# Performance work log

Measured on AMD Instinct MI355X. Metric: run time of the kernel, lower is better.

Reference implementation:

```python
import jax, jax.numpy as jnp
import numpy as np

N_CLASSES = 5
N_SAMPLES = 512
D_EMB = 512


def setup_inputs() -> dict:
    key = jax.random.key(0)
    k1, k2, k3 = jax.random.split(key, 3)
    prediction = jax.random.normal(k1, (N_SAMPLES, D_EMB), dtype=jnp.float32)
    target = jax.random.randint(k2, (N_SAMPLES,), 0, N_CLASSES)
    # learnable_map=None -> all learnable, init = inverse_softplus(0.5 + 0.5*U[0,1))
    t = 0.5 + 0.5 * jax.random.uniform(k3, (N_CLASSES - 1,), dtype=jnp.float32)
    distances_raw = jnp.log(jnp.exp(t) - 1.0)  # inverse softplus (t < 20 always)
    return {"prediction": prediction, "distances_raw": distances_raw, "target": target}


def reference(prediction, distances_raw, target):
    n = prediction.shape[0]
    eps = 1e-8  # torch F.cosine_similarity eps
    xn = prediction / jnp.maximum(jnp.linalg.norm(prediction, axis=1, keepdims=True), eps)
    cos = xn @ xn.T  # [i, j] pairwise cosine similarity

    same = target[:, None] == target[None, :]          # label_diff <= 0
    positives = same & ~jnp.eye(n, dtype=bool)          # same label, not self
    negatives = ~same                                   # different label

    # ordinal class positions from softplus-parameterized gaps
    pos_d = jax.nn.softplus(distances_raw)
    class_pos = jnp.concatenate([jnp.zeros(1, dtype=pos_d.dtype), jnp.cumsum(pos_d)])
    cp = class_pos[target]
    margins = jnp.where(negatives, jnp.abs(cp[:, None] - cp[None, :]), 0.0)  # [i, j]

    # Original loop over anchor-positive columns k:
    #   n_pair_loss[k][i, j] = -cos[i, k] + cos[i, j] + margins[i, j]
    #   valid iff positives[i, k] and negatives[i, j]; invalid -> relu(-inf)=0
    base = cos + margins                                # [i, j]
    diff = base[:, None, :] - cos[:, :, None]           # [i, k, j]
    val = jnp.where(negatives[:, None, :], jax.nn.relu(diff), 0.0)
    s = jnp.where(positives, val.sum(axis=2), 0.0)      # [i, k]
    negcount = negatives.sum(axis=1)                    # [i]
    cnt = jnp.where(positives, negcount[:, None], 0)    # loss_mask2
    L = s / jnp.maximum(cnt, 1)                         # per (anchor i, positive k)

    # mean over nonzero entries (mean_n_pair_loss[mean_n_pair_loss != 0].mean())
    nz = (L != 0.0).sum()
    return L.sum() / jnp.maximum(nz, 1).astype(L.dtype)
```

## Files before the change

kernel.cpp:

```cpp
#include <hip/hip_runtime.h>
#include <math.h>

#define NS 512
#define DE 512
#define NCL 5
#define KSPLIT 16
#define PART_ELEMS (KSPLIT * NS * NS)


__global__ __launch_bounds__(256, 1) void k_gemm(const float* __restrict__ pred,
                                                 float* __restrict__ part,
                                                 float* __restrict__ dpart,
                                                 unsigned int* __restrict__ ctrl) {
    const int tid = threadIdx.x;
    if (blockIdx.x == 0 && blockIdx.y == 0 && blockIdx.z == 0 && tid < 4) ctrl[tid] = 0u;

    __shared__ float4 As4[128][8];
    __shared__ float4 Bs4[128][8];

    const int row0 = blockIdx.y * 128, col0 = blockIdx.x * 128;
    const int z = blockIdx.z;
    const int kz0 = z * 32;

    const int lr = tid >> 1;
    const int sbase = (tid & 1) * 4;
    const int swz = (lr >> 3) & 7;
    const float4* gA = (const float4*)&pred[(row0 + lr) * DE + kz0];
    const float4* gB = (const float4*)&pred[(col0 + lr) * DE + kz0];
#pragma unroll
    for (int q = 0; q < 4; q++) {
        int s = sbase + q;
        As4[lr][s ^ swz] = gA[s];
        Bs4[lr][s ^ swz] = gB[s];
    }
    __syncthreads();

    const int tx = tid & 15, ty = tid >> 4;
    const int aswz = ty & 7, bswz = tx & 7;
    float acc[8][8] = {};

#pragma unroll
    for (int q = 0; q < 8; q++) {
        float4 b4[8];
#pragma unroll
        for (int c = 0; c < 8; c++) b4[c] = Bs4[tx * 8 + c][q ^ bswz];
#pragma unroll
        for (int rr = 0; rr < 2; rr++) {
            float4 a4[4];
#pragma unroll
            for (int r = 0; r < 4; r++) a4[r] = As4[ty * 8 + rr * 4 + r][q ^ aswz];
#pragma unroll
            for (int r = 0; r < 4; r++) {
#pragma unroll
                for (int c = 0; c < 8; c++) {
                    float v = acc[rr * 4 + r][c];
                    v = fmaf(a4[r].x, b4[c].x, v);
                    v = fmaf(a4[r].y, b4[c].y, v);
                    v = fmaf(a4[r].z, b4[c].z, v);
                    v = fmaf(a4[r].w, b4[c].w, v);
                    acc[rr * 4 + r][c] = v;
                }
            }
        }
    }

    float* op = part + (size_t)z * NS * NS;
#pragma unroll
    for (int m = 0; m < 8; m++) {
        float4 o0 = make_float4(acc[m][0], acc[m][1], acc[m][2], acc[m][3]);
        float4 o1 = make_float4(acc[m][4], acc[m][5], acc[m][6], acc[m][7]);
        float* dst = &op[(row0 + ty * 8 + m) * NS + col0 + tx * 8];
        *(float4*)dst = o0;
        *(float4*)(dst + 4) = o1;
    }

    if (blockIdx.x == blockIdx.y && ty == tx) {
#pragma unroll
        for (int m = 0; m < 8; m++)
            dpart[z * NS + row0 + ty * 8 + m] = acc[m][m];
    }
}

__global__ __launch_bounds__(256) void k_loss(const float* __restrict__ part,
                                              const float* __restrict__ dpart,
                                              const int* __restrict__ target,
                                              const float* __restrict__ draw,
                                              unsigned int* __restrict__ ctrl,
                                              float* __restrict__ out) {
    const int b = blockIdx.x;
    const int tid = threadIdx.x;
    const int iA = b, iB = b + 256;

    __shared__ float4 v4sA[NS / 4], v4sB[NS / 4];
    __shared__ float  ckA[NS], ckB[NS];
    __shared__ float  rn_s[NS];
    __shared__ int    pkA[NS], pkB[NS];
    __shared__ float  spart[NS * 17];
    __shared__ float  redf[256];
    __shared__ int    redi[256];
    __shared__ unsigned int pcA, pcB;

    float* gsum = (float*)ctrl;
    unsigned int* gnz    = ctrl + 1;
    unsigned int* ticket = ctrl + 2;

    float2 d2 = make_float2(0.0f, 0.0f);
#pragma unroll
    for (int z = 0; z < KSPLIT; z++) {
        float2 t2 = ((const float2*)&dpart[z * NS])[tid];
        d2.x += t2.x; d2.y += t2.y;
    }
    const float rn0 = 1.0f / fmaxf(sqrtf(d2.x), 1e-8f);
    const float rn1 = 1.0f / fmaxf(sqrtf(d2.y), 1e-8f);
    const int j0 = tid * 2;
    rn_s[j0] = rn0; rn_s[j0 + 1] = rn1;
    if (tid == 0) { pcA = 0u; pcB = 0u; }

    float2 gA = make_float2(0.0f, 0.0f), gB = make_float2(0.0f, 0.0f);
#pragma unroll
    for (int z = 0; z < KSPLIT; z++) {
        const float* base = part + (size_t)z * NS * NS;
        float2 tA = ((const float2*)&base[(size_t)iA * NS])[tid];
        float2 tB = ((const float2*)&base[(size_t)iB * NS])[tid];
        gA.x += tA.x; gA.y += tA.y;
        gB.x += tB.x; gB.y += tB.y;
    }

    float cp[NCL];
    cp[0] = 0.0f;
#pragma unroll
    for (int c = 0; c < NCL - 1; c++) cp[c + 1] = cp[c] + log1pf(expf(draw[c]));
    const int tiA = target[iA], tiB = target[iB];
    const float cpA = cp[tiA], cpB = cp[tiB];
    __syncthreads();

    const float rniA = rn_s[iA], rniB = rn_s[iB];
    const int tj0 = target[j0], tj1 = target[j0 + 1];
    const float cpj0 = cp[tj0], cpj1 = cp[tj1];

    {
        float c0 = gA.x * rniA * rn0;
        float c1 = gA.y * rniA * rn1;
        bool n0 = (tj0 != tiA), n1 = (tj1 != tiA);
        ckA[j0] = c0; ckA[j0 + 1] = c1;
        ((float2*)v4sA)[tid] = make_float2(n0 ? (c0 + fabsf(cpA - cpj0)) : -1e30f,
                                           n1 ? (c1 + fabsf(cpA - cpj1)) : -1e30f);
        if (!n0 && j0 != iA)     pkA[atomicAdd(&pcA, 1u)] = j0;
        if (!n1 && j0 + 1 != iA) pkA[atomicAdd(&pcA, 1u)] = j0 + 1;
        redi[tid] = ((n0 ? 1 : 0) + (n1 ? 1 : 0));
    }
    {
        float c0 = gB.x * rniB * rn0;
        float c1 = gB.y * rniB * rn1;
        bool n0 = (tj0 != tiB), n1 = (tj1 != tiB);
        ckB[j0] = c0; ckB[j0 + 1] = c1;
        ((float2*)v4sB)[tid] = make_float2(n0 ? (c0 + fabsf(cpB - cpj0)) : -1e30f,
                                           n1 ? (c1 + fabsf(cpB - cpj1)) : -1e30f);
        if (!n0 && j0 != iB)     pkB[atomicAdd(&pcB, 1u)] = j0;
        if (!n1 && j0 + 1 != iB) pkB[atomicAdd(&pcB, 1u)] = j0 + 1;
        redi[tid] += ((n0 ? 1 : 0) + (n1 ? 1 : 0)) << 16;
    }
    __syncthreads();
    for (int s = 128; s > 0; s >>= 1) {
        if (tid < s) redi[tid] += redi[tid + s];
        __syncthreads();
    }
    const int negA = redi[0] & 0xffff;
    const int negB = redi[0] >> 16;
    const unsigned int nposA = pcA, nposB = pcB;
    __syncthreads();

    const int kl = tid & 15, jc = tid >> 4;
    const float denA = (float)(negA > 1 ? negA : 1);
    const float denB = (float)(negB > 1 ? negB : 1);
    float contrib = 0.0f;
    int nzc = 0;

    {
        float4 vj[8];
#pragma unroll
        for (int t = 0; t < 8; t++) vj[t] = v4sA[jc * 8 + t];
        for (unsigned int p = kl; p < nposA; p += 16) {
            const float ckp = ckA[pkA[p]];
            float s0 = 0.0f, s1 = 0.0f;
#pragma unroll
            for (int t = 0; t < 8; t++) {
                float4 w = vj[t];
                s0 += fmaxf(w.x - ckp, 0.0f) + fmaxf(w.y - ckp, 0.0f);
                s1 += fmaxf(w.z - ckp, 0.0f) + fmaxf(w.w - ckp, 0.0f);
            }
            spart[p * 17 + jc] = s0 + s1;
        }
        __syncthreads();
        for (unsigned int p = tid; p < nposA; p += 256) {
            float s = 0.0f;
#pragma unroll
            for (int q = 0; q < 16; q++) s += spart[p * 17 + q];
            contrib += s / denA;
            if (s != 0.0f) nzc++;
        }
        __syncthreads();
    }
    {
        float4 vj[8];
#pragma unroll
        for (int t = 0; t < 8; t++) vj[t] = v4sB[jc * 8 + t];
        for (unsigned int p = kl; p < nposB; p += 16) {
            const float ckp = ckB[pkB[p]];
            float s0 = 0.0f, s1 = 0.0f;
#pragma unroll
            for (int t = 0; t < 8; t++) {
                float4 w = vj[t];
                s0 += fmaxf(w.x - ckp, 0.0f) + fmaxf(w.y - ckp, 0.0f);
                s1 += fmaxf(w.z - ckp, 0.0f) + fmaxf(w.w - ckp, 0.0f);
            }
            spart[p * 17 + jc] = s0 + s1;
        }
        __syncthreads();
        for (unsigned int p = tid; p < nposB; p += 256) {
            float s = 0.0f;
#pragma unroll
            for (int q = 0; q < 16; q++) s += spart[p * 17 + q];
            contrib += s / denB;
            if (s != 0.0f) nzc++;
        }
    }

    redf[tid] = contrib;
    redi[tid] = nzc;
    __syncthreads();
    for (int s = 128; s > 0; s >>= 1) {
        if (tid < s) { redf[tid] += redf[tid + s]; redi[tid] += redi[tid + s]; }
        __syncthreads();
    }
    if (tid == 0) {
        if (redf[0] != 0.0f || redi[0] != 0) {
            atomicAdd(gsum, redf[0]);
            atomicAdd(gnz, (unsigned int)redi[0]);
        }
        __threadfence();
        unsigned int t = atomicAdd(ticket, 1u);
        if (t == (unsigned int)(gridDim.x - 1)) {
            float s = atomicAdd(gsum, 0.0f);
            unsigned int n = atomicAdd(gnz, 0u);
            out[0] = s / (float)(n > 1u ? n : 1u);
        }
    }
}

extern "C" void kernel_launch(void* const* d_in, const int* in_sizes, int n_in,
                              void* d_out, int out_size, void* d_ws, size_t ws_size,
                              hipStream_t stream) {
    const float* pred   = (const float*)d_in[0];
    const float* draw   = (const float*)d_in[1];
    const int*   target = (const int*)d_in[2];
    float* out = (float*)d_out;

    float* ws    = (float*)d_ws;
    float* part  = ws;
    float* dpart = ws + PART_ELEMS;
    unsigned int* ctrl = (unsigned int*)(dpart + KSPLIT * NS);

    hipLaunchKernelGGL(k_gemm, dim3(4, 4, KSPLIT), dim3(256), 0, stream,
                       pred, part, dpart, ctrl);
    hipLaunchKernelGGL(k_loss, dim3(256), dim3(256), 0, stream,
                       part, dpart, target, draw, ctrl, out);
}
```

Baseline: 91.22 us.

## Fuse GEMM and loss kernels with a software grid barrier

```diff
diff --git a/kernel.cpp b/kernel.cpp
--- a/kernel.cpp
+++ b/kernel.cpp
@@ -6,103 +6,113 @@
 #define NCL 5
 #define KSPLIT 16
 #define PART_ELEMS (KSPLIT * NS * NS)
-
-
-__global__ __launch_bounds__(256, 1) void k_gemm(const float* __restrict__ pred,
-                                                 float* __restrict__ part,
-                                                 float* __restrict__ dpart,
-                                                 unsigned int* __restrict__ ctrl) {
+#define NBLK 256
+
+
+union SMem {
+    struct { float4 As4[128][8]; float4 Bs4[128][8]; } g;
+    struct {
+        float4 v4sA[NS / 4], v4sB[NS / 4];
+        float  ckA[NS], ckB[NS];
+        float  rn_s[NS];
+        int    pkA[NS], pkB[NS];
+        float  spart[NS * 17];
+        float  redf[256];
+        int    redi[256];
+        unsigned int pcA, pcB;
+    } l;
+};
+
+__global__ __launch_bounds__(256) void k_fused(const float* __restrict__ pred,
+                                               const int* __restrict__ target,
+                                               const float* __restrict__ draw,
+                                               float* __restrict__ part,
+                                               float* __restrict__ dpart,
+                                               unsigned int* __restrict__ ctrl,
+                                               float* __restrict__ out) {
+    __shared__ SMem sm;
     const int tid = threadIdx.x;
-    if (blockIdx.x == 0 && blockIdx.y == 0 && blockIdx.z == 0 && tid < 4) ctrl[tid] = 0u;
-
-    __shared__ float4 As4[128][8];
-    __shared__ float4 Bs4[128][8];
-
-    const int row0 = blockIdx.y * 128, col0 = blockIdx.x * 128;
-    const int z = blockIdx.z;
-    const int kz0 = z * 32;
-
-    const int lr = tid >> 1;
-    const int sbase = (tid & 1) * 4;
-    const int swz = (lr >> 3) & 7;
-    const float4* gA = (const float4*)&pred[(row0 + lr) * DE + kz0];
-    const float4* gB = (const float4*)&pred[(col0 + lr) * DE + kz0];
-#pragma unroll
-    for (int q = 0; q < 4; q++) {
-        int s = sbase + q;
-        As4[lr][s ^ swz] = gA[s];
-        Bs4[lr][s ^ swz] = gB[s];
-    }
-    __syncthreads();
-
-    const int tx = tid & 15, ty = tid >> 4;
-    const int aswz = ty & 7, bswz = tx & 7;
-    float acc[8][8] = {};
-
-#pragma unroll
-    for (int q = 0; q < 8; q++) {
-        float4 b4[8];
-#pragma unroll
-        for (int c = 0; c < 8; c++) b4[c] = Bs4[tx * 8 + c][q ^ bswz];
-#pragma unroll
-        for (int rr = 0; rr < 2; rr++) {
-            float4 a4[4];
-#pragma unroll
-            for (int r = 0; r < 4; r++) a4[r] = As4[ty * 8 + rr * 4 + r][q ^ aswz];
-#pragma unroll
-            for (int r = 0; r < 4; r++) {
-#pragma unroll
-                for (int c = 0; c < 8; c++) {
-                    float v = acc[rr * 4 + r][c];
-                    v = fmaf(a4[r].x, b4[c].x, v);
-                    v = fmaf(a4[r].y, b4[c].y, v);
-                    v = fmaf(a4[r].z, b4[c].z, v);
-                    v = fmaf(a4[r].w, b4[c].w, v);
-                    acc[rr * 4 + r][c] = v;
+    const int b = blockIdx.x;
+
+    {
+        const int t = b >> 4, z = b & 15;
+        const int row0 = (t >> 2) * 128, col0 = (t & 3) * 128;
+        const int kz0 = z * 32;
+
+        const int lr = tid >> 1;
+        const int sbase = (tid & 1) * 4;
+        const int swz = (lr >> 3) & 7;
+        const float4* gA = (const float4*)&pred[(row0 + lr) * DE + kz0];
+        const float4* gB = (const float4*)&pred[(col0 + lr) * DE + kz0];
+#pragma unroll
+        for (int q = 0; q < 4; q++) {
+            int s = sbase + q;
+            sm.g.As4[lr][s ^ swz] = gA[s];
+            sm.g.Bs4[lr][s ^ swz] = gB[s];
+        }
+        __syncthreads();
+
+        const int tx = tid & 15, ty = tid >> 4;
+        const int aswz = ty & 7, bswz = tx & 7;
+        float acc[8][8] = {};
+#pragma unroll
+        for (int q = 0; q < 8; q++) {
+            float4 b4[8];
+#pragma unroll
+            for (int c = 0; c < 8; c++) b4[c] = sm.g.Bs4[tx * 8 + c][q ^ bswz];
+#pragma unroll
+            for (int rr = 0; rr < 2; rr++) {
+                float4 a4[4];
+#pragma unroll
+                for (int r = 0; r < 4; r++) a4[r] = sm.g.As4[ty * 8 + rr * 4 + r][q ^ aswz];
+#pragma unroll
+                for (int r = 0; r < 4; r++) {
+#pragma unroll
+                    for (int c = 0; c < 8; c++) {
+                        float v = acc[rr * 4 + r][c];
+                        v = fmaf(a4[r].x, b4[c].x, v);
+                        v = fmaf(a4[r].y, b4[c].y, v);
+                        v = fmaf(a4[r].z, b4[c].z, v);
+                        v = fmaf(a4[r].w, b4[c].w, v);
+                        acc[rr * 4 + r][c] = v;
+                    }
                 }
             }
         }
-    }
-
-    float* op = part + (size_t)z * NS * NS;
-#pragma unroll
-    for (int m = 0; m < 8; m++) {
-        float4 o0 = make_float4(acc[m][0], acc[m][1], acc[m][2], acc[m][3]);
-        float4 o1 = make_float4(acc[m][4], acc[m][5], acc[m][6], acc[m][7]);
-        float* dst = &op[(row0 + ty * 8 + m) * NS + col0 + tx * 8];
-        *(float4*)dst = o0;
-        *(float4*)(dst + 4) = o1;
-    }
-
-    if (blockIdx.x == blockIdx.y && ty == tx) {
-#pragma unroll
-        for (int m = 0; m < 8; m++)
-            dpart[z * NS + row0 + ty * 8 + m] = acc[m][m];
-    }
-}
-
-__global__ __launch_bounds__(256) void k_loss(const float* __restrict__ part,
-                                              const float* __restrict__ dpart,
-                                              const int* __restrict__ target,
-                                              const float* __restrict__ draw,
-                                              unsigned int* __restrict__ ctrl,
-                                              float* __restrict__ out) {
-    const int b = blockIdx.x;
-    const int tid = threadIdx.x;
+        float* op = part + (size_t)z * NS * NS;
+#pragma unroll
+        for (int m = 0; m < 8; m++) {
+            float4 o0 = make_float4(acc[m][0], acc[m][1], acc[m][2], acc[m][3]);
+            float4 o1 = make_float4(acc[m][4], acc[m][5], acc[m][6], acc[m][7]);
+            float* dst = &op[(row0 + ty * 8 + m) * NS + col0 + tx * 8];
+            *(float4*)dst = o0;
+            *(float4*)(dst + 4) = o1;
+        }
+        if ((t >> 2) == (t & 3) && ty == tx) {
+#pragma unroll
+            for (int m = 0; m < 8; m++)
+                dpart[z * NS + row0 + ty * 8 + m] = acc[m][m];
+        }
+    }
+
+    {
+        __threadfence();
+        __syncthreads();
+        if (tid == 0) {
+            unsigned int* bar = ctrl + 2;
+            atomicAdd(bar, 1u);
+            while (__hip_atomic_load(bar, __ATOMIC_ACQUIRE,
+                                     __HIP_MEMORY_SCOPE_AGENT) < (unsigned int)NBLK)
+                __builtin_amdgcn_s_sleep(4);
+        }
+        __syncthreads();
+        __threadfence();
+    }
+
     const int iA = b, iB = b + 256;
-
-    __shared__ float4 v4sA[NS / 4], v4sB[NS / 4];
-    __shared__ float  ckA[NS], ckB[NS];
-    __shared__ float  rn_s[NS];
-    __shared__ int    pkA[NS], pkB[NS];
-    __shared__ float  spart[NS * 17];
-    __shared__ float  redf[256];
-    __shared__ int    redi[256];
-    __shared__ unsigned int pcA, pcB;
-
     float* gsum = (float*)ctrl;
     unsigned int* gnz    = ctrl + 1;
-    unsigned int* ticket = ctrl + 2;
+    unsigned int* ticket = ctrl + 3;
 
     float2 d2 = make_float2(0.0f, 0.0f);
 #pragma unroll
@@ -113,17 +123,17 @@
     const float rn0 = 1.0f / fmaxf(sqrtf(d2.x), 1e-8f);
     const float rn1 = 1.0f / fmaxf(sqrtf(d2.y), 1e-8f);
     const int j0 = tid * 2;
-    rn_s[j0] = rn0; rn_s[j0 + 1] = rn1;
-    if (tid == 0) { pcA = 0u; pcB = 0u; }
-
-    float2 gA = make_float2(0.0f, 0.0f), gB = make_float2(0.0f, 0.0f);
+    sm.l.rn_s[j0] = rn0; sm.l.rn_s[j0 + 1] = rn1;
+    if (tid == 0) { sm.l.pcA = 0u; sm.l.pcB = 0u; }
+
+    float2 gA2 = make_float2(0.0f, 0.0f), gB2 = make_float2(0.0f, 0.0f);
 #pragma unroll
     for (int z = 0; z < KSPLIT; z++) {
         const float* base = part + (size_t)z * NS * NS;
         float2 tA = ((const float2*)&base[(size_t)iA * NS])[tid];
         float2 tB = ((const float2*)&base[(size_t)iB * NS])[tid];
-        gA.x += tA.x; gA.y += tA.y;
-        gB.x += tB.x; gB.y += tB.y;
+        gA2.x += tA.x; gA2.y += tA.y;
+        gB2.x += tB.x; gB2.y += tB.y;
     }
 
     float cp[NCL];
@@ -134,40 +144,40 @@
     const float cpA = cp[tiA], cpB = cp[tiB];
     __syncthreads();
 
-    const float rniA = rn_s[iA], rniB = rn_s[iB];
+    const float rniA = sm.l.rn_s[iA], rniB = sm.l.rn_s[iB];
     const int tj0 = target[j0], tj1 = target[j0 + 1];
     const float cpj0 = cp[tj0], cpj1 = cp[tj1];
 
     {
-        float c0 = gA.x * rniA * rn0;
-        float c1 = gA.y * rniA * rn1;
+        float c0 = gA2.x * rniA * rn0;
+        float c1 = gA2.y * rniA * rn1;
         bool n0 = (tj0 != tiA), n1 = (tj1 != tiA);
-        ckA[j0] = c0; ckA[j0 + 1] = c1;
-        ((float2*)v4sA)[tid] = make_float2(n0 ? (c0 + fabsf(cpA - cpj0)) : -1e30f,
-                                           n1 ? (c1 + fabsf(cpA - cpj1)) : -1e30f);
-        if (!n0 && j0 != iA)     pkA[atomicAdd(&pcA, 1u)] = j0;
-        if (!n1 && j0 + 1 != iA) pkA[atomicAdd(&pcA, 1u)] = j0 + 1;
-        redi[tid] = ((n0 ? 1 : 0) + (n1 ? 1 : 0));
-    }
-    {
-        float c0 = gB.x * rniB * rn0;
-        float c1 = gB.y * rniB * rn1;
+        sm.l.ckA[j0] = c0; sm.l.ckA[j0 + 1] = c1;
+        ((float2*)sm.l.v4sA)[tid] = make_float2(n0 ? (c0 + fabsf(cpA - cpj0)) : -1e30f,
+                                                n1 ? (c1 + fabsf(cpA - cpj1)) : -1e30f);
+        if (!n0 && j0 != iA)     sm.l.pkA[atomicAdd(&sm.l.pcA, 1u)] = j0;
+        if (!n1 && j0 + 1 != iA) sm.l.pkA[atomicAdd(&sm.l.pcA, 1u)] = j0 + 1;
+        sm.l.redi[tid] = ((n0 ? 1 : 0) + (n1 ? 1 : 0));
+    }
+    {
+        float c0 = gB2.x * rniB * rn0;
+        float c1 = gB2.y * rniB * rn1;
         bool n0 = (tj0 != tiB), n1 = (tj1 != tiB);
-        ckB[j0] = c0; ckB[j0 + 1] = c1;
-        ((float2*)v4sB)[tid] = make_float2(n0 ? (c0 + fabsf(cpB - cpj0)) : -1e30f,
-                                           n1 ? (c1 + fabsf(cpB - cpj1)) : -1e30f);
-        if (!n0 && j0 != iB)     pkB[atomicAdd(&pcB, 1u)] = j0;
-        if (!n1 && j0 + 1 != iB) pkB[atomicAdd(&pcB, 1u)] = j0 + 1;
-        redi[tid] += ((n0 ? 1 : 0) + (n1 ? 1 : 0)) << 16;
+        sm.l.ckB[j0] = c0; sm.l.ckB[j0 + 1] = c1;
+        ((float2*)sm.l.v4sB)[tid] = make_float2(n0 ? (c0 + fabsf(cpB - cpj0)) : -1e30f,
+                                                n1 ? (c1 + fabsf(cpB - cpj1)) : -1e30f);
+        if (!n0 && j0 != iB)     sm.l.pkB[atomicAdd(&sm.l.pcB, 1u)] = j0;
+        if (!n1 && j0 + 1 != iB) sm.l.pkB[atomicAdd(&sm.l.pcB, 1u)] = j0 + 1;
+        sm.l.redi[tid] += ((n0 ? 1 : 0) + (n1 ? 1 : 0)) << 16;
     }
     __syncthreads();
     for (int s = 128; s > 0; s >>= 1) {
-        if (tid < s) redi[tid] += redi[tid + s];
-        __syncthreads();
-    }
-    const int negA = redi[0] & 0xffff;
-    const int negB = redi[0] >> 16;
-    const unsigned int nposA = pcA, nposB = pcB;
+        if (tid < s) sm.l.redi[tid] += sm.l.redi[tid + s];
+        __syncthreads();
+    }
+    const int negA = sm.l.redi[0] & 0xffff;
+    const int negB = sm.l.redi[0] >> 16;
+    const unsigned int nposA = sm.l.pcA, nposB = sm.l.pcB;
     __syncthreads();
 
     const int kl = tid & 15, jc = tid >> 4;
@@ -179,9 +189,9 @@
     {
         float4 vj[8];
 #pragma unroll
-        for (int t = 0; t < 8; t++) vj[t] = v4sA[jc * 8 + t];
+        for (int t = 0; t < 8; t++) vj[t] = sm.l.v4sA[jc * 8 + t];
         for (unsigned int p = kl; p < nposA; p += 16) {
-            const float ckp = ckA[pkA[p]];
+            const float ckp = sm.l.ckA[sm.l.pkA[p]];
             float s0 = 0.0f, s1 = 0.0f;
 #pragma unroll
             for (int t = 0; t < 8; t++) {
@@ -189,13 +199,13 @@
                 s0 += fmaxf(w.x - ckp, 0.0f) + fmaxf(w.y - ckp, 0.0f);
                 s1 += fmaxf(w.z - ckp, 0.0f) + fmaxf(w.w - ckp, 0.0f);
             }
-            spart[p * 17 + jc] = s0 + s1;
+            sm.l.spart[p * 17 + jc] = s0 + s1;
         }
         __syncthreads();
         for (unsigned int p = tid; p < nposA; p += 256) {
             float s = 0.0f;
 #pragma unroll
-            for (int q = 0; q < 16; q++) s += spart[p * 17 + q];
+            for (int q = 0; q < 16; q++) s += sm.l.spart[p * 17 + q];
             contrib += s / denA;
             if (s != 0.0f) nzc++;
         }
@@ -204,9 +214,9 @@
     {
         float4 vj[8];
 #pragma unroll
-        for (int t = 0; t < 8; t++) vj[t] = v4sB[jc * 8 + t];
+        for (int t = 0; t < 8; t++) vj[t] = sm.l.v4sB[jc * 8 + t];
         for (unsigned int p = kl; p < nposB; p += 16) {
-            const float ckp = ckB[pkB[p]];
+            const float ckp = sm.l.ckB[sm.l.pkB[p]];
             float s0 = 0.0f, s1 = 0.0f;
 #pragma unroll
             for (int t = 0; t < 8; t++) {
@@ -214,33 +224,33 @@
                 s0 += fmaxf(w.x - ckp, 0.0f) + fmaxf(w.y - ckp, 0.0f);
                 s1 += fmaxf(w.z - ckp, 0.0f) + fmaxf(w.w - ckp, 0.0f);
             }
-            spart[p * 17 + jc] = s0 + s1;
+            sm.l.spart[p * 17 + jc] = s0 + s1;
         }
         __syncthreads();
         for (unsigned int p = tid; p < nposB; p += 256) {
             float s = 0.0f;
 #pragma unroll
-            for (int q = 0; q < 16; q++) s += spart[p * 17 + q];
+            for (int q = 0; q < 16; q++) s += sm.l.spart[p * 17 + q];
             contrib += s / denB;
             if (s != 0.0f) nzc++;
         }
     }
 
-    redf[tid] = contrib;
-    redi[tid] = nzc;
+    sm.l.redf[tid] = contrib;
+    sm.l.redi[tid] = nzc;
     __syncthreads();
     for (int s = 128; s > 0; s >>= 1) {
-        if (tid < s) { redf[tid] += redf[tid + s]; redi[tid] += redi[tid + s]; }
+        if (tid < s) { sm.l.redf[tid] += sm.l.redf[tid + s]; sm.l.redi[tid] += sm.l.redi[tid + s]; }
         __syncthreads();
     }
     if (tid == 0) {
-        if (redf[0] != 0.0f || redi[0] != 0) {
-            atomicAdd(gsum, redf[0]);
-            atomicAdd(gnz, (unsigned int)redi[0]);
+        if (sm.l.redf[0] != 0.0f || sm.l.redi[0] != 0) {
+            atomicAdd(gsum, sm.l.redf[0]);
+            atomicAdd(gnz, (unsigned int)sm.l.redi[0]);
         }
         __threadfence();
         unsigned int t = atomicAdd(ticket, 1u);
-        if (t == (unsigned int)(gridDim.x - 1)) {
+        if (t == (unsigned int)(NBLK - 1)) {
             float s = atomicAdd(gsum, 0.0f);
             unsigned int n = atomicAdd(gnz, 0u);
             out[0] = s / (float)(n > 1u ? n : 1u);
@@ -261,8 +271,7 @@
     float* dpart = ws + PART_ELEMS;
     unsigned int* ctrl = (unsigned int*)(dpart + KSPLIT * NS);
 
-    hipLaunchKernelGGL(k_gemm, dim3(4, 4, KSPLIT), dim3(256), 0, stream,
-                       pred, part, dpart, ctrl);
-    hipLaunchKernelGGL(k_loss, dim3(256), dim3(256), 0, stream,
-                       part, dpart, target, draw, ctrl, out);
+    hipMemsetAsync(ctrl, 0, 4 * sizeof(unsigned int), stream);
+    hipLaunchKernelGGL(k_fused, dim3(NBLK), dim3(256), 0, stream,
+                       pred, target, draw, part, dpart, ctrl, out);
 }
```

Measured after the change: 156.1 us. 71.2% more time.

## Fuse split-K GEMM into loss kernel computing cosine rows per block

Applied to the files above, without the earlier changes.

```diff
diff --git a/kernel.cpp b/kernel.cpp
--- a/kernel.cpp
+++ b/kernel.cpp
@@ -4,96 +4,22 @@
 #define NS 512
 #define DE 512
 #define NCL 5
-#define KSPLIT 16
-#define PART_ELEMS (KSPLIT * NS * NS)
-
-
-__global__ __launch_bounds__(256, 1) void k_gemm(const float* __restrict__ pred,
-                                                 float* __restrict__ part,
-                                                 float* __restrict__ dpart,
-                                                 unsigned int* __restrict__ ctrl) {
-    const int tid = threadIdx.x;
-    if (blockIdx.x == 0 && blockIdx.y == 0 && blockIdx.z == 0 && tid < 4) ctrl[tid] = 0u;
-
-    __shared__ float4 As4[128][8];
-    __shared__ float4 Bs4[128][8];
-
-    const int row0 = blockIdx.y * 128, col0 = blockIdx.x * 128;
-    const int z = blockIdx.z;
-    const int kz0 = z * 32;
-
-    const int lr = tid >> 1;
-    const int sbase = (tid & 1) * 4;
-    const int swz = (lr >> 3) & 7;
-    const float4* gA = (const float4*)&pred[(row0 + lr) * DE + kz0];
-    const float4* gB = (const float4*)&pred[(col0 + lr) * DE + kz0];
-#pragma unroll
-    for (int q = 0; q < 4; q++) {
-        int s = sbase + q;
-        As4[lr][s ^ swz] = gA[s];
-        Bs4[lr][s ^ swz] = gB[s];
-    }
-    __syncthreads();
-
-    const int tx = tid & 15, ty = tid >> 4;
-    const int aswz = ty & 7, bswz = tx & 7;
-    float acc[8][8] = {};
-
-#pragma unroll
-    for (int q = 0; q < 8; q++) {
-        float4 b4[8];
-#pragma unroll
-        for (int c = 0; c < 8; c++) b4[c] = Bs4[tx * 8 + c][q ^ bswz];
-#pragma unroll
-        for (int rr = 0; rr < 2; rr++) {
-            float4 a4[4];
-#pragma unroll
-            for (int r = 0; r < 4; r++) a4[r] = As4[ty * 8 + rr * 4 + r][q ^ aswz];
-#pragma unroll
-            for (int r = 0; r < 4; r++) {
-#pragma unroll
-                for (int c = 0; c < 8; c++) {
-                    float v = acc[rr * 4 + r][c];
-                    v = fmaf(a4[r].x, b4[c].x, v);
-                    v = fmaf(a4[r].y, b4[c].y, v);
-                    v = fmaf(a4[r].z, b4[c].z, v);
-                    v = fmaf(a4[r].w, b4[c].w, v);
-                    acc[rr * 4 + r][c] = v;
-                }
-            }
-        }
-    }
-
-    float* op = part + (size_t)z * NS * NS;
-#pragma unroll
-    for (int m = 0; m < 8; m++) {
-        float4 o0 = make_float4(acc[m][0], acc[m][1], acc[m][2], acc[m][3]);
-        float4 o1 = make_float4(acc[m][4], acc[m][5], acc[m][6], acc[m][7]);
-        float* dst = &op[(row0 + ty * 8 + m) * NS + col0 + tx * 8];
-        *(float4*)dst = o0;
-        *(float4*)(dst + 4) = o1;
-    }
-
-    if (blockIdx.x == blockIdx.y && ty == tx) {
-#pragma unroll
-        for (int m = 0; m < 8; m++)
-            dpart[z * NS + row0 + ty * 8 + m] = acc[m][m];
-    }
-}
-
-__global__ __launch_bounds__(256) void k_loss(const float* __restrict__ part,
-                                              const float* __restrict__ dpart,
-                                              const int* __restrict__ target,
-                                              const float* __restrict__ draw,
-                                              unsigned int* __restrict__ ctrl,
-                                              float* __restrict__ out) {
+#define NBLK 256
+
+
+__global__ __launch_bounds__(256) void k_all(const float* __restrict__ pred,
+                                             const int* __restrict__ target,
+                                             const float* __restrict__ draw,
+                                             unsigned int* __restrict__ ctrl,
+                                             float* __restrict__ out) {
     const int b = blockIdx.x;
     const int tid = threadIdx.x;
     const int iA = b, iB = b + 256;
 
+    __shared__ float4 sA4[DE / 4], sB4[DE / 4];
+    __shared__ float  rn_s[NS];
     __shared__ float4 v4sA[NS / 4], v4sB[NS / 4];
     __shared__ float  ckA[NS], ckB[NS];
-    __shared__ float  rn_s[NS];
     __shared__ int    pkA[NS], pkB[NS];
     __shared__ float  spart[NS * 17];
     __shared__ float  redf[256];
@@ -104,27 +30,44 @@
     unsigned int* gnz    = ctrl + 1;
     unsigned int* ticket = ctrl + 2;
 
-    float2 d2 = make_float2(0.0f, 0.0f);
-#pragma unroll
-    for (int z = 0; z < KSPLIT; z++) {
-        float2 t2 = ((const float2*)&dpart[z * NS])[tid];
-        d2.x += t2.x; d2.y += t2.y;
-    }
-    const float rn0 = 1.0f / fmaxf(sqrtf(d2.x), 1e-8f);
-    const float rn1 = 1.0f / fmaxf(sqrtf(d2.y), 1e-8f);
+    if (tid < 128) sA4[tid]       = ((const float4*)&pred[(size_t)iA * DE])[tid];
+    else           sB4[tid - 128] = ((const float4*)&pred[(size_t)iB * DE])[tid - 128];
+    if (tid == 0) { pcA = 0u; pcB = 0u; }
+    __syncthreads();
+
     const int j0 = tid * 2;
+    const float4* r0 = (const float4*)&pred[(size_t)j0 * DE];
+    const float4* r1 = (const float4*)&pred[(size_t)(j0 + 1) * DE];
+
+    float4 aA0 = {0,0,0,0}, aA1 = {0,0,0,0};
+    float4 aB0 = {0,0,0,0}, aB1 = {0,0,0,0};
+    float4 aS0 = {0,0,0,0}, aS1 = {0,0,0,0};
+#pragma unroll 4
+    for (int k = 0; k < DE / 4; k++) {
+        float4 x0 = r0[k], x1 = r1[k];
+        float4 a = sA4[k], bb = sB4[k];
+        aA0.x = fmaf(x0.x, a.x, aA0.x);  aA0.y = fmaf(x0.y, a.y, aA0.y);
+        aA0.z = fmaf(x0.z, a.z, aA0.z);  aA0.w = fmaf(x0.w, a.w, aA0.w);
+        aA1.x = fmaf(x1.x, a.x, aA1.x);  aA1.y = fmaf(x1.y, a.y, aA1.y);
+        aA1.z = fmaf(x1.z, a.z, aA1.z);  aA1.w = fmaf(x1.w, a.w, aA1.w);
+        aB0.x = fmaf(x0.x, bb.x, aB0.x); aB0.y = fmaf(x0.y, bb.y, aB0.y);
+        aB0.z = fmaf(x0.z, bb.z, aB0.z); aB0.w = fmaf(x0.w, bb.w, aB0.w);
+        aB1.x = fmaf(x1.x, bb.x, aB1.x); aB1.y = fmaf(x1.y, bb.y, aB1.y);
+        aB1.z = fmaf(x1.z, bb.z, aB1.z); aB1.w = fmaf(x1.w, bb.w, aB1.w);
+        aS0.x = fmaf(x0.x, x0.x, aS0.x); aS0.y = fmaf(x0.y, x0.y, aS0.y);
+        aS0.z = fmaf(x0.z, x0.z, aS0.z); aS0.w = fmaf(x0.w, x0.w, aS0.w);
+        aS1.x = fmaf(x1.x, x1.x, aS1.x); aS1.y = fmaf(x1.y, x1.y, aS1.y);
+        aS1.z = fmaf(x1.z, x1.z, aS1.z); aS1.w = fmaf(x1.w, x1.w, aS1.w);
+    }
+    const float dA0 = aA0.x + aA0.y + aA0.z + aA0.w;
+    const float dA1 = aA1.x + aA1.y + aA1.z + aA1.w;
+    const float dB0 = aB0.x + aB0.y + aB0.z + aB0.w;
+    const float dB1 = aB1.x + aB1.y + aB1.z + aB1.w;
+    const float ns0 = aS0.x + aS0.y + aS0.z + aS0.w;
+    const float ns1 = aS1.x + aS1.y + aS1.z + aS1.w;
+    const float rn0 = 1.0f / fmaxf(sqrtf(ns0), 1e-8f);
+    const float rn1 = 1.0f / fmaxf(sqrtf(ns1), 1e-8f);
     rn_s[j0] = rn0; rn_s[j0 + 1] = rn1;
-    if (tid == 0) { pcA = 0u; pcB = 0u; }
-
-    float2 gA = make_float2(0.0f, 0.0f), gB = make_float2(0.0f, 0.0f);
-#pragma unroll
-    for (int z = 0; z < KSPLIT; z++) {
-        const float* base = part + (size_t)z * NS * NS;
-        float2 tA = ((const float2*)&base[(size_t)iA * NS])[tid];
-        float2 tB = ((const float2*)&base[(size_t)iB * NS])[tid];
-        gA.x += tA.x; gA.y += tA.y;
-        gB.x += tB.x; gB.y += tB.y;
-    }
 
     float cp[NCL];
     cp[0] = 0.0f;
@@ -132,15 +75,15 @@
     for (int c = 0; c < NCL - 1; c++) cp[c + 1] = cp[c] + log1pf(expf(draw[c]));
     const int tiA = target[iA], tiB = target[iB];
     const float cpA = cp[tiA], cpB = cp[tiB];
-    __syncthreads();
-
-    const float rniA = rn_s[iA], rniB = rn_s[iB];
     const int tj0 = target[j0], tj1 = target[j0 + 1];
     const float cpj0 = cp[tj0], cpj1 = cp[tj1];
-
-    {
-        float c0 = gA.x * rniA * rn0;
-        float c1 = gA.y * rniA * rn1;
+    __syncthreads();
+
+    const float rniA = rn_s[iA], rniB = rn_s[iB];
+
+    {
+        float c0 = dA0 * rniA * rn0;
+        float c1 = dA1 * rniA * rn1;
         bool n0 = (tj0 != tiA), n1 = (tj1 != tiA);
         ckA[j0] = c0; ckA[j0 + 1] = c1;
         ((float2*)v4sA)[tid] = make_float2(n0 ? (c0 + fabsf(cpA - cpj0)) : -1e30f,
@@ -150,8 +93,8 @@
         redi[tid] = ((n0 ? 1 : 0) + (n1 ? 1 : 0));
     }
     {
-        float c0 = gB.x * rniB * rn0;
-        float c1 = gB.y * rniB * rn1;
+        float c0 = dB0 * rniB * rn0;
+        float c1 = dB1 * rniB * rn1;
         bool n0 = (tj0 != tiB), n1 = (tj1 != tiB);
         ckB[j0] = c0; ckB[j0 + 1] = c1;
         ((float2*)v4sB)[tid] = make_float2(n0 ? (c0 + fabsf(cpB - cpj0)) : -1e30f,
@@ -240,7 +183,7 @@
         }
         __threadfence();
         unsigned int t = atomicAdd(ticket, 1u);
-        if (t == (unsigned int)(gridDim.x - 1)) {
+        if (t == (unsigned int)(NBLK - 1)) {
             float s = atomicAdd(gsum, 0.0f);
             unsigned int n = atomicAdd(gnz, 0u);
             out[0] = s / (float)(n > 1u ? n : 1u);
@@ -256,13 +199,9 @@
     const int*   target = (const int*)d_in[2];
     float* out = (float*)d_out;
 
-    float* ws    = (float*)d_ws;
-    float* part  = ws;
-    float* dpart = ws + PART_ELEMS;
-    unsigned int* ctrl = (unsigned int*)(dpart + KSPLIT * NS);
-
-    hipLaunchKernelGGL(k_gemm, dim3(4, 4, KSPLIT), dim3(256), 0, stream,
-                       pred, part, dpart, ctrl);
-    hipLaunchKernelGGL(k_loss, dim3(256), dim3(256), 0, stream,
-                       part, dpart, target, draw, ctrl, out);
+    unsigned int* ctrl = (unsigned int*)d_ws;
+
+    hipMemsetAsync(ctrl, 0, 4 * sizeof(unsigned int), stream);
+    hipLaunchKernelGGL(k_all, dim3(NBLK), dim3(256), 0, stream,
+                       pred, target, draw, ctrl, out);
 }
```

Result: slower. 104.2 us (+14.2%).
